# Performance work log

Hardware: AMD Instinct MI355X
Metric: run time of the kernel (lower is better)

## Reference

```python
import jax, jax.numpy as jnp
import numpy as np

B, N, F_IN, F_OUT = 128, 512, 128, 64
ALPHA = 0.2        # LeakyReLU slope for attention logits
GAIN = 1.414       # xavier gain used in the torch module
NEG_INF = -9e15    # mask value from the torch code


def _xavier_uniform(key, shape, gain):
    fan_in, fan_out = shape[0], shape[1]
    limit = gain * np.sqrt(6.0 / (fan_in + fan_out))
    return jax.random.uniform(key, shape, jnp.float32, -limit, limit)


def setup_inputs() -> dict:
    key = jax.random.key(0)
    k1, k2, k3, k4 = jax.random.split(key, 4)
    input_hid = jax.random.normal(k1, (B, N, F_IN), jnp.float32)
    adj = jax.random.randint(k2, (B, N, N), 0, 2, jnp.int32)  # 0/1 adjacency
    W = _xavier_uniform(k3, (F_IN, F_OUT), GAIN)
    a = _xavier_uniform(k4, (2 * F_OUT, 1), GAIN)
    return {"input_hid": input_hid, "adj": adj, "W": W, "a": a}


def reference(input_hid, adj, W, a):
    # h: [B, N, F_OUT]
    h = jnp.matmul(input_hid, W)
    # Standard GAT decomposition of the concat-repeat construction:
    # e[b,i,j] = leakyrelu( [h_i || h_j] @ a ) = leakyrelu( h_i@a_src + h_j@a_dst )
    a_src = a[:F_OUT, 0]   # applies to the repeated-row (i) half
    a_dst = a[F_OUT:, 0]   # applies to the tiled (j) half
    s = jnp.einsum('bnf,f->bn', h, a_src)  # [B, N]
    t = jnp.einsum('bnf,f->bn', h, a_dst)  # [B, N]
    e = jax.nn.leaky_relu(s[:, :, None] + t[:, None, :], ALPHA)  # [B, N, N]
    e = jnp.where(adj > 0, e, NEG_INF)
    att = jax.nn.softmax(e, axis=2)        # softmax over neighbors j
    h_prime = jnp.matmul(att, h)           # [B, N, F_OUT]
    # concat=True -> F.leaky_relu with torch default slope 0.01
    return jax.nn.leaky_relu(h_prime, 0.01)
```

## Files before the change

kernel.cpp:

```cpp
#include <hip/hip_runtime.h>
#include <stdint.h>

#define B_   128
#define N_   512
#define FIN  128
#define FOUT 64

using bf16x8 = __attribute__((ext_vector_type(8))) short;
using f32x4  = __attribute__((ext_vector_type(4))) float;

__device__ inline unsigned short f2bf(float x) {
    union { float f; uint32_t u; } c; c.f = x;
    uint32_t u = c.u;
    return (unsigned short)((u + 0x7FFFu + ((u >> 16) & 1u)) >> 16);
}

__global__ __launch_bounds__(256) void k_h(const float* __restrict__ X,
                                           const float* __restrict__ W,
                                           const float* __restrict__ a,
                                           uint16_t* __restrict__ htT,
                                           float* __restrict__ s,
                                           float* __restrict__ t) {
    __shared__ bf16x8 ax[32 * 64];
    __shared__ bf16x8 wl[16 * 64];

    const int b  = blockIdx.x >> 2;
    const int j0 = (blockIdx.x & 3) * 128;
    const int tid = threadIdx.x;
    const int w = tid >> 6, lane = tid & 63;
    const int q = lane >> 4, m = lane & 15;

#pragma unroll
    for (int nt = 0; nt < 4; ++nt) {
        bf16x8 fr;
#pragma unroll
        for (int u = 0; u < 8; ++u)
            fr[u] = (short)f2bf(W[(w * 32 + q * 8 + u) * FOUT + nt * 16 + m]);
        wl[(w * 4 + nt) * 64 + lane] = fr;
    }

    const float* xb = X + ((size_t)(b * N_) + j0) * FIN;
#pragma unroll
    for (int i = 0; i < 8; ++i) {
        int pi = i * 4 + w, rt = pi >> 2, ks = pi & 3;
        const float* src = xb + (size_t)(rt * 16 + m) * FIN + ks * 32 + q * 8;
        float4 v0 = *(const float4*)src;
        float4 v1 = *(const float4*)(src + 4);
        bf16x8 fr;
        fr[0] = (short)f2bf(v0.x); fr[1] = (short)f2bf(v0.y);
        fr[2] = (short)f2bf(v0.z); fr[3] = (short)f2bf(v0.w);
        fr[4] = (short)f2bf(v1.x); fr[5] = (short)f2bf(v1.y);
        fr[6] = (short)f2bf(v1.z); fr[7] = (short)f2bf(v1.w);
        ax[pi * 64 + lane] = fr;
    }
    __syncthreads();

    float asv[4], adv[4];
#pragma unroll
    for (int nt = 0; nt < 4; ++nt) {
        asv[nt] = a[nt * 16 + m];
        adv[nt] = a[FOUT + nt * 16 + m];
    }

    for (int rl = 0; rl < 2; ++rl) {
        const int rt = w + rl * 4;
        f32x4 acc[4] = {{0.f,0.f,0.f,0.f},{0.f,0.f,0.f,0.f},
                        {0.f,0.f,0.f,0.f},{0.f,0.f,0.f,0.f}};
#pragma unroll
        for (int ks = 0; ks < 4; ++ks) {
            bf16x8 af = ax[(rt * 4 + ks) * 64 + lane];
#pragma unroll
            for (int nt = 0; nt < 4; ++nt)
                acc[nt] = __builtin_amdgcn_mfma_f32_16x16x32_bf16(
                    af, wl[(ks * 4 + nt) * 64 + lane], acc[nt], 0, 0, 0);
        }

        float ps[4], pt[4];
#pragma unroll
        for (int r = 0; r < 4; ++r) {
            float vs = 0.f, vt = 0.f;
#pragma unroll
            for (int nt = 0; nt < 4; ++nt) {
                vs += acc[nt][r] * asv[nt];
                vt += acc[nt][r] * adv[nt];
            }
            vs += __shfl_xor(vs, 1, 64); vs += __shfl_xor(vs, 2, 64);
            vs += __shfl_xor(vs, 4, 64); vs += __shfl_xor(vs, 8, 64);
            vt += __shfl_xor(vt, 1, 64); vt += __shfl_xor(vt, 2, 64);
            vt += __shfl_xor(vt, 4, 64); vt += __shfl_xor(vt, 8, 64);
            ps[r] = vs; pt[r] = vt;
        }
        if (m < 4) {
            float vs = (m == 0) ? ps[0] : (m == 1) ? ps[1] : (m == 2) ? ps[2] : ps[3];
            float vt = (m == 0) ? pt[0] : (m == 1) ? pt[1] : (m == 2) ? pt[2] : pt[3];
            int row = j0 + rt * 16 + q * 4 + m;
            s[b * N_ + row] = vs;
            t[b * N_ + row] = vt;
        }

#pragma unroll
        for (int nt = 0; nt < 4; ++nt) {
            uint32_t d0 = (uint32_t)f2bf(acc[nt][0]) | ((uint32_t)f2bf(acc[nt][1]) << 16);
            uint32_t d1 = (uint32_t)f2bf(acc[nt][2]) | ((uint32_t)f2bf(acc[nt][3]) << 16);
            uint2 dd; dd.x = d0; dd.y = d1;
            *(uint2*)(htT + (size_t)(b * FOUT + nt * 16 + m) * N_ + j0 + rt * 16 + q * 4) = dd;
        }
    }
}

__global__ __launch_bounds__(256) void k_attn(const int*    __restrict__ adj,
                                              const uint16_t* __restrict__ htT,
                                              const float*  __restrict__ s,
                                              const float*  __restrict__ t,
                                              float*        __restrict__ out) {
    __shared__ bf16x8 hstage[64 * 64];
    __shared__ float  tsh[N_];

    const int b  = blockIdx.x >> 2;
    const int i0 = (blockIdx.x & 3) * 128;
    const int tid = threadIdx.x;
    const int w = tid >> 6, lane = tid & 63;
    const int q = lane >> 4, m = lane & 15;

    const uint16_t* hb = htT + (size_t)b * FOUT * N_;
#pragma unroll
    for (int i = 0; i < 16; ++i) {
        int pi = i * 4 + w, ks = pi >> 2, nt = pi & 3;
        bf16x8 v = *(const bf16x8*)(hb + (size_t)(nt * 16 + m) * N_ + ks * 32 + q * 8);
        hstage[pi * 64 + lane] = v;
    }
    *(float2*)&tsh[tid * 2] = *(const float2*)(t + b * N_ + tid * 2);
    __syncthreads();

    const int ir0 = i0 + w * 16 + m;
    const int ir1 = ir0 + 64;
    const float s0 = s[b * N_ + ir0];
    const float s1 = s[b * N_ + ir1];
    const int* ar0 = adj + ((size_t)(b * N_) + ir0) * N_;
    const int* ar1 = adj + ((size_t)(b * N_) + ir1) * N_;

    f32x4 acc0[4] = {{0.f,0.f,0.f,0.f},{0.f,0.f,0.f,0.f},
                     {0.f,0.f,0.f,0.f},{0.f,0.f,0.f,0.f}};
    f32x4 acc1[4] = {{0.f,0.f,0.f,0.f},{0.f,0.f,0.f,0.f},
                     {0.f,0.f,0.f,0.f},{0.f,0.f,0.f,0.f}};
    float ls0 = 0.f, ls1 = 0.f;

    int4 c00 = *(const int4*)(ar0 + q * 8);
    int4 c01 = *(const int4*)(ar0 + q * 8 + 4);
    int4 c10 = *(const int4*)(ar1 + q * 8);
    int4 c11 = *(const int4*)(ar1 + q * 8 + 4);

    for (int ks = 0; ks < 16; ++ks) {
        const int jn = ((ks < 15) ? ks + 1 : ks) * 32 + q * 8;
        int4 n00 = *(const int4*)(ar0 + jn);
        int4 n01 = *(const int4*)(ar0 + jn + 4);
        int4 n10 = *(const int4*)(ar1 + jn);
        int4 n11 = *(const int4*)(ar1 + jn + 4);

        const int jb = ks * 32 + q * 8;
        float tj[8];
#pragma unroll
        for (int u = 0; u < 8; ++u) tj[u] = tsh[jb + u];

        int av0[8] = {c00.x, c00.y, c00.z, c00.w, c01.x, c01.y, c01.z, c01.w};
        int av1[8] = {c10.x, c10.y, c10.z, c10.w, c11.x, c11.y, c11.z, c11.w};
        bf16x8 af0, af1;
#pragma unroll
        for (int u = 0; u < 8; ++u) {
            float e0 = s0 + tj[u];
            e0 = fmaxf(e0, 0.2f * e0);
            float p0 = (av0[u] > 0) ? __expf(e0) : 0.0f;
            ls0 += p0;
            af0[u] = (short)f2bf(p0);
            float e1 = s1 + tj[u];
            e1 = fmaxf(e1, 0.2f * e1);
            float p1 = (av1[u] > 0) ? __expf(e1) : 0.0f;
            ls1 += p1;
            af1[u] = (short)f2bf(p1);
        }

        bf16x8 bf0 = hstage[(ks * 4 + 0) * 64 + lane];
        bf16x8 bf1 = hstage[(ks * 4 + 1) * 64 + lane];
        bf16x8 bf2 = hstage[(ks * 4 + 2) * 64 + lane];
        bf16x8 bf3 = hstage[(ks * 4 + 3) * 64 + lane];

        acc0[0] = __builtin_amdgcn_mfma_f32_16x16x32_bf16(af0, bf0, acc0[0], 0, 0, 0);
        acc0[1] = __builtin_amdgcn_mfma_f32_16x16x32_bf16(af0, bf1, acc0[1], 0, 0, 0);
        acc0[2] = __builtin_amdgcn_mfma_f32_16x16x32_bf16(af0, bf2, acc0[2], 0, 0, 0);
        acc0[3] = __builtin_amdgcn_mfma_f32_16x16x32_bf16(af0, bf3, acc0[3], 0, 0, 0);
        acc1[0] = __builtin_amdgcn_mfma_f32_16x16x32_bf16(af1, bf0, acc1[0], 0, 0, 0);
        acc1[1] = __builtin_amdgcn_mfma_f32_16x16x32_bf16(af1, bf1, acc1[1], 0, 0, 0);
        acc1[2] = __builtin_amdgcn_mfma_f32_16x16x32_bf16(af1, bf2, acc1[2], 0, 0, 0);
        acc1[3] = __builtin_amdgcn_mfma_f32_16x16x32_bf16(af1, bf3, acc1[3], 0, 0, 0);

        c00 = n00; c01 = n01; c10 = n10; c11 = n11;
    }

    ls0 += __shfl_xor(ls0, 16, 64);
    ls0 += __shfl_xor(ls0, 32, 64);
    ls1 += __shfl_xor(ls1, 16, 64);
    ls1 += __shfl_xor(ls1, 32, 64);

#pragma unroll
    for (int reg = 0; reg < 4; ++reg) {
        float lr0 = __shfl(ls0, q * 4 + reg, 64);
        float lr1 = __shfl(ls1, q * 4 + reg, 64);
        float inv0 = 1.0f / lr0, inv1 = 1.0f / lr1;
        int orow0 = i0 + w * 16 + q * 4 + reg;
        size_t ob0 = ((size_t)(b * N_) + orow0) * FOUT + m;
        size_t ob1 = ob0 + (size_t)64 * FOUT;
#pragma unroll
        for (int nt = 0; nt < 4; ++nt) {
            float v0 = acc0[nt][reg] * inv0; v0 = fmaxf(v0, 0.01f * v0);
            float v1 = acc1[nt][reg] * inv1; v1 = fmaxf(v1, 0.01f * v1);
            out[ob0 + nt * 16] = v0;
            out[ob1 + nt * 16] = v1;
        }
    }
}

extern "C" void kernel_launch(void* const* d_in, const int* in_sizes, int n_in,
                              void* d_out, int out_size, void* d_ws, size_t ws_size,
                              hipStream_t stream) {
    const float* X   = (const float*)d_in[0];
    const int*   adj = (const int*)  d_in[1];
    const float* W   = (const float*)d_in[2];
    const float* a   = (const float*)d_in[3];
    float* out = (float*)d_out;

    uint16_t* htT = (uint16_t*)d_ws;
    float* s = (float*)(htT + (size_t)B_ * FOUT * N_);
    float* t = s + B_ * N_;

    k_h<<<B_ * 4, 256, 0, stream>>>(X, W, a, htT, s, t);
    k_attn<<<B_ * 4, 256, 0, stream>>>(adj, htT, s, t, out);
}
```

Before: 232.9 us.

## Drop LDS staging, use hardware bf16 pack and exp2, remap attention blocks

Replaces the software bf16 rounding with v_cvt_pk_bf16_f32 and __expf with raw v_exp_f32, folding log2(e) into the attention vector a so the exp2 result stays exact. Both kernels stop staging X and htT in shared memory and load fragments straight from global memory into MFMA operands. The attention grid is remapped with a blockIdx permutation, and launch bounds now request 4 blocks per CU. The aim is less ALU work per element and lower LDS use for higher occupancy, at the cost of more global and L2 traffic for the h fragments.

New measurement: 231.7 us. Within noise of the previous version (-0.5%).

```diff
diff --git a/kernel.cpp b/kernel.cpp
--- a/kernel.cpp
+++ b/kernel.cpp
@@ -9,19 +9,25 @@
 using bf16x8 = __attribute__((ext_vector_type(8))) short;
 using f32x4  = __attribute__((ext_vector_type(4))) float;
 
-__device__ inline unsigned short f2bf(float x) {
-    union { float f; uint32_t u; } c; c.f = x;
-    uint32_t u = c.u;
-    return (unsigned short)((u + 0x7FFFu + ((u >> 16) & 1u)) >> 16);
-}
-
-__global__ __launch_bounds__(256) void k_h(const float* __restrict__ X,
-                                           const float* __restrict__ W,
-                                           const float* __restrict__ a,
-                                           uint16_t* __restrict__ htT,
-                                           float* __restrict__ s,
-                                           float* __restrict__ t) {
-    __shared__ bf16x8 ax[32 * 64];
+__device__ inline uint32_t cvt_pk_bf16(float lo, float hi) {
+    uint32_t r;
+    asm("v_cvt_pk_bf16_f32 %0, %1, %2" : "=v"(r) : "v"(lo), "v"(hi));
+    return r;
+}
+__device__ inline float exp2_fast(float x) {
+    float r;
+    asm("v_exp_f32 %0, %1" : "=v"(r) : "v"(x));
+    return r;
+}
+
+union bfpack { bf16x8 v; uint32_t w4[4]; };
+
+__global__ __launch_bounds__(256, 4) void k_h(const float* __restrict__ X,
+                                              const float* __restrict__ W,
+                                              const float* __restrict__ a,
+                                              uint16_t* __restrict__ htT,
+                                              float* __restrict__ s,
+                                              float* __restrict__ t) {
     __shared__ bf16x8 wl[16 * 64];
 
     const int b  = blockIdx.x >> 2;
@@ -32,47 +38,48 @@
 
 #pragma unroll
     for (int nt = 0; nt < 4; ++nt) {
-        bf16x8 fr;
+        float wv[8];
 #pragma unroll
         for (int u = 0; u < 8; ++u)
-            fr[u] = (short)f2bf(W[(w * 32 + q * 8 + u) * FOUT + nt * 16 + m]);
-        wl[(w * 4 + nt) * 64 + lane] = fr;
+            wv[u] = W[(w * 32 + q * 8 + u) * FOUT + nt * 16 + m];
+        bfpack fr;
+        fr.w4[0] = cvt_pk_bf16(wv[0], wv[1]);
+        fr.w4[1] = cvt_pk_bf16(wv[2], wv[3]);
+        fr.w4[2] = cvt_pk_bf16(wv[4], wv[5]);
+        fr.w4[3] = cvt_pk_bf16(wv[6], wv[7]);
+        wl[(w * 4 + nt) * 64 + lane] = fr.v;
+    }
+    __syncthreads();
+
+    const float LOG2E = 1.44269504088896340736f;
+    float asv[4], adv[4];
+#pragma unroll
+    for (int nt = 0; nt < 4; ++nt) {
+        asv[nt] = a[nt * 16 + m] * LOG2E;
+        adv[nt] = a[FOUT + nt * 16 + m] * LOG2E;
     }
 
     const float* xb = X + ((size_t)(b * N_) + j0) * FIN;
-#pragma unroll
-    for (int i = 0; i < 8; ++i) {
-        int pi = i * 4 + w, rt = pi >> 2, ks = pi & 3;
-        const float* src = xb + (size_t)(rt * 16 + m) * FIN + ks * 32 + q * 8;
-        float4 v0 = *(const float4*)src;
-        float4 v1 = *(const float4*)(src + 4);
-        bf16x8 fr;
-        fr[0] = (short)f2bf(v0.x); fr[1] = (short)f2bf(v0.y);
-        fr[2] = (short)f2bf(v0.z); fr[3] = (short)f2bf(v0.w);
-        fr[4] = (short)f2bf(v1.x); fr[5] = (short)f2bf(v1.y);
-        fr[6] = (short)f2bf(v1.z); fr[7] = (short)f2bf(v1.w);
-        ax[pi * 64 + lane] = fr;
-    }
-    __syncthreads();
-
-    float asv[4], adv[4];
-#pragma unroll
-    for (int nt = 0; nt < 4; ++nt) {
-        asv[nt] = a[nt * 16 + m];
-        adv[nt] = a[FOUT + nt * 16 + m];
-    }
-
+
+#pragma unroll
     for (int rl = 0; rl < 2; ++rl) {
         const int rt = w + rl * 4;
         f32x4 acc[4] = {{0.f,0.f,0.f,0.f},{0.f,0.f,0.f,0.f},
                         {0.f,0.f,0.f,0.f},{0.f,0.f,0.f,0.f}};
 #pragma unroll
         for (int ks = 0; ks < 4; ++ks) {
-            bf16x8 af = ax[(rt * 4 + ks) * 64 + lane];
+            const float* src = xb + (size_t)(rt * 16 + m) * FIN + ks * 32 + q * 8;
+            float4 v0 = *(const float4*)src;
+            float4 v1 = *(const float4*)(src + 4);
+            bfpack af;
+            af.w4[0] = cvt_pk_bf16(v0.x, v0.y);
+            af.w4[1] = cvt_pk_bf16(v0.z, v0.w);
+            af.w4[2] = cvt_pk_bf16(v1.x, v1.y);
+            af.w4[3] = cvt_pk_bf16(v1.z, v1.w);
 #pragma unroll
             for (int nt = 0; nt < 4; ++nt)
                 acc[nt] = __builtin_amdgcn_mfma_f32_16x16x32_bf16(
-                    af, wl[(ks * 4 + nt) * 64 + lane], acc[nt], 0, 0, 0);
+                    af.v, wl[(ks * 4 + nt) * 64 + lane], acc[nt], 0, 0, 0);
         }
 
         float ps[4], pt[4];
@@ -100,38 +107,32 @@
 
 #pragma unroll
         for (int nt = 0; nt < 4; ++nt) {
-            uint32_t d0 = (uint32_t)f2bf(acc[nt][0]) | ((uint32_t)f2bf(acc[nt][1]) << 16);
-            uint32_t d1 = (uint32_t)f2bf(acc[nt][2]) | ((uint32_t)f2bf(acc[nt][3]) << 16);
-            uint2 dd; dd.x = d0; dd.y = d1;
+            uint2 dd;
+            dd.x = cvt_pk_bf16(acc[nt][0], acc[nt][1]);
+            dd.y = cvt_pk_bf16(acc[nt][2], acc[nt][3]);
             *(uint2*)(htT + (size_t)(b * FOUT + nt * 16 + m) * N_ + j0 + rt * 16 + q * 4) = dd;
         }
     }
 }
 
-__global__ __launch_bounds__(256) void k_attn(const int*    __restrict__ adj,
-                                              const uint16_t* __restrict__ htT,
-                                              const float*  __restrict__ s,
-                                              const float*  __restrict__ t,
-                                              float*        __restrict__ out) {
-    __shared__ bf16x8 hstage[64 * 64];
-    __shared__ float  tsh[N_];
-
-    const int b  = blockIdx.x >> 2;
-    const int i0 = (blockIdx.x & 3) * 128;
+__global__ __launch_bounds__(256, 4) void k_attn(const int*    __restrict__ adj,
+                                                 const uint16_t* __restrict__ htT,
+                                                 const float*  __restrict__ s,
+                                                 const float*  __restrict__ t,
+                                                 float*        __restrict__ out) {
+    __shared__ float tsh[N_];
+
+    const int wg = (blockIdx.x & 7) * 64 + (blockIdx.x >> 3);
+    const int b  = wg >> 2;
+    const int i0 = (wg & 3) * 128;
     const int tid = threadIdx.x;
     const int w = tid >> 6, lane = tid & 63;
     const int q = lane >> 4, m = lane & 15;
 
-    const uint16_t* hb = htT + (size_t)b * FOUT * N_;
-#pragma unroll
-    for (int i = 0; i < 16; ++i) {
-        int pi = i * 4 + w, ks = pi >> 2, nt = pi & 3;
-        bf16x8 v = *(const bf16x8*)(hb + (size_t)(nt * 16 + m) * N_ + ks * 32 + q * 8);
-        hstage[pi * 64 + lane] = v;
-    }
     *(float2*)&tsh[tid * 2] = *(const float2*)(t + b * N_ + tid * 2);
     __syncthreads();
 
+    const uint16_t* hb = htT + (size_t)b * FOUT * N_;
     const int ir0 = i0 + w * 16 + m;
     const int ir1 = ir0 + 64;
     const float s0 = s[b * N_ + ir0];
@@ -157,6 +158,12 @@
         int4 n10 = *(const int4*)(ar1 + jn);
         int4 n11 = *(const int4*)(ar1 + jn + 4);
 
+        const uint16_t* hks = hb + ks * 32 + q * 8;
+        bf16x8 bf0 = *(const bf16x8*)(hks + (size_t)( 0 + m) * N_);
+        bf16x8 bf1 = *(const bf16x8*)(hks + (size_t)(16 + m) * N_);
+        bf16x8 bf2 = *(const bf16x8*)(hks + (size_t)(32 + m) * N_);
+        bf16x8 bf3 = *(const bf16x8*)(hks + (size_t)(48 + m) * N_);
+
         const int jb = ks * 32 + q * 8;
         float tj[8];
 #pragma unroll
@@ -164,34 +171,34 @@
 
         int av0[8] = {c00.x, c00.y, c00.z, c00.w, c01.x, c01.y, c01.z, c01.w};
         int av1[8] = {c10.x, c10.y, c10.z, c10.w, c11.x, c11.y, c11.z, c11.w};
-        bf16x8 af0, af1;
-#pragma unroll
-        for (int u = 0; u < 8; ++u) {
-            float e0 = s0 + tj[u];
-            e0 = fmaxf(e0, 0.2f * e0);
-            float p0 = (av0[u] > 0) ? __expf(e0) : 0.0f;
-            ls0 += p0;
-            af0[u] = (short)f2bf(p0);
-            float e1 = s1 + tj[u];
-            e1 = fmaxf(e1, 0.2f * e1);
-            float p1 = (av1[u] > 0) ? __expf(e1) : 0.0f;
-            ls1 += p1;
-            af1[u] = (short)f2bf(p1);
-        }
-
-        bf16x8 bf0 = hstage[(ks * 4 + 0) * 64 + lane];
-        bf16x8 bf1 = hstage[(ks * 4 + 1) * 64 + lane];
-        bf16x8 bf2 = hstage[(ks * 4 + 2) * 64 + lane];
-        bf16x8 bf3 = hstage[(ks * 4 + 3) * 64 + lane];
-
-        acc0[0] = __builtin_amdgcn_mfma_f32_16x16x32_bf16(af0, bf0, acc0[0], 0, 0, 0);
-        acc0[1] = __builtin_amdgcn_mfma_f32_16x16x32_bf16(af0, bf1, acc0[1], 0, 0, 0);
-        acc0[2] = __builtin_amdgcn_mfma_f32_16x16x32_bf16(af0, bf2, acc0[2], 0, 0, 0);
-        acc0[3] = __builtin_amdgcn_mfma_f32_16x16x32_bf16(af0, bf3, acc0[3], 0, 0, 0);
-        acc1[0] = __builtin_amdgcn_mfma_f32_16x16x32_bf16(af1, bf0, acc1[0], 0, 0, 0);
-        acc1[1] = __builtin_amdgcn_mfma_f32_16x16x32_bf16(af1, bf1, acc1[1], 0, 0, 0);
-        acc1[2] = __builtin_amdgcn_mfma_f32_16x16x32_bf16(af1, bf2, acc1[2], 0, 0, 0);
-        acc1[3] = __builtin_amdgcn_mfma_f32_16x16x32_bf16(af1, bf3, acc1[3], 0, 0, 0);
+
+        bfpack pk0, pk1;
+#pragma unroll
+        for (int up = 0; up < 4; ++up) {
+            float e; float x;
+            e = s0 + tj[2 * up];     e = fmaxf(e, 0.2f * e); x = exp2_fast(e);
+            float pa0 = (av0[2 * up] > 0) ? x : 0.0f;
+            e = s0 + tj[2 * up + 1]; e = fmaxf(e, 0.2f * e); x = exp2_fast(e);
+            float pb0 = (av0[2 * up + 1] > 0) ? x : 0.0f;
+            ls0 += pa0 + pb0;
+            pk0.w4[up] = cvt_pk_bf16(pa0, pb0);
+
+            e = s1 + tj[2 * up];     e = fmaxf(e, 0.2f * e); x = exp2_fast(e);
+            float pa1 = (av1[2 * up] > 0) ? x : 0.0f;
+            e = s1 + tj[2 * up + 1]; e = fmaxf(e, 0.2f * e); x = exp2_fast(e);
+            float pb1 = (av1[2 * up + 1] > 0) ? x : 0.0f;
+            ls1 += pa1 + pb1;
+            pk1.w4[up] = cvt_pk_bf16(pa1, pb1);
+        }
+
+        acc0[0] = __builtin_amdgcn_mfma_f32_16x16x32_bf16(pk0.v, bf0, acc0[0], 0, 0, 0);
+        acc0[1] = __builtin_amdgcn_mfma_f32_16x16x32_bf16(pk0.v, bf1, acc0[1], 0, 0, 0);
+        acc0[2] = __builtin_amdgcn_mfma_f32_16x16x32_bf16(pk0.v, bf2, acc0[2], 0, 0, 0);
+        acc0[3] = __builtin_amdgcn_mfma_f32_16x16x32_bf16(pk0.v, bf3, acc0[3], 0, 0, 0);
+        acc1[0] = __builtin_amdgcn_mfma_f32_16x16x32_bf16(pk1.v, bf0, acc1[0], 0, 0, 0);
+        acc1[1] = __builtin_amdgcn_mfma_f32_16x16x32_bf16(pk1.v, bf1, acc1[1], 0, 0, 0);
+        acc1[2] = __builtin_amdgcn_mfma_f32_16x16x32_bf16(pk1.v, bf2, acc1[2], 0, 0, 0);
+        acc1[3] = __builtin_amdgcn_mfma_f32_16x16x32_bf16(pk1.v, bf3, acc1[3], 0, 0, 0);
 
         c00 = n00; c01 = n01; c10 = n10; c11 = n11;
     }
```
